# Performance work log

Measured on AMD Instinct MI355X. Metric: run time of the kernel, lower is better.

Reference implementation:

```python
import jax, jax.numpy as jnp
import numpy as np
from jax.scipy.linalg import expm

UNITS = 128  # input last dim = UNITS + 1 (state + time column)


def setup_inputs() -> dict:
    key = jax.random.key(0)
    k1, k2 = jax.random.split(key)
    # [B, units+1]: first `units` cols are the state x, last col is time t
    inputs = jax.random.uniform(k1, (4096, UNITS + 1), dtype=jnp.float32)
    # posterior sample w of size 2*units-1 (diag params + skew params)
    params = jax.random.normal(k2, (2 * UNITS - 1,), dtype=jnp.float32)
    return {"inputs": inputs, "params": params}


def _vec_to_K(params, units):
    # sigma = -softplus(p[:units])**2  -> (negative) diagonal of generator
    sigma = -jax.nn.softplus(params[:units]) ** 2
    # ceta = -p[units:2*units-1]      -> skew super/sub-diagonal
    ceta = -params[units:2 * units - 1]
    # K = diag(sigma) + M - M^T where M = pad(diag(ceta)) is the superdiagonal
    return jnp.diag(sigma) + jnp.diag(ceta, 1) - jnp.diag(ceta, -1)


def reference(inputs, params):
    units = inputs.shape[-1] - 1
    K = _vec_to_K(params, units)                       # [n, n]
    t = inputs[..., -1]                                # [B]
    # kernel_b = expm(t_b * K)  -> batched matrix exponential [B, n, n]
    kernel = jax.vmap(expm)(t[:, None, None] * K)
    # out_b = x_b @ kernel_b
    out = jnp.einsum('bn,bnm->bm', inputs[..., :units], kernel)
    return out
```

## Files before the change

kernel.cpp:

```cpp
#include <hip/hip_runtime.h>
#include <math.h>

#define UNITS 128


__global__ __launch_bounds__(256) void expv_kernel(
    const float* __restrict__ inputs,
    const float* __restrict__ params,
    float* __restrict__ out,
    int B)
{
    const int gid  = blockIdx.x * blockDim.x + threadIdx.x;
    const int wave = gid >> 6;
    const int lane = gid & 63;
    if (wave >= B) return;

    const int i0 = lane * 2;

    const float p0 = params[i0];
    const float p1 = params[i0 + 1];
    const float sp0 = fmaxf(p0, 0.f) + log1pf(expf(-fabsf(p0)));
    const float sp1 = fmaxf(p1, 0.f) + log1pf(expf(-fabsf(p1)));
    const float sig0 = -sp0 * sp0;
    const float sig1 = -sp1 * sp1;
    const float ce0 = -params[UNITS + i0];
    const float ce1 = (lane < 63) ? -params[UNITS + i0 + 1] : 0.f;
    const float ced = (lane > 0)  ? -params[UNITS + i0 - 1] : 0.f;

    const float* row = inputs + (size_t)wave * (UNITS + 1);
    const float x0 = row[i0];
    const float x1 = row[i0 + 1];
    const float t  = row[UNITS];

    const float a0 = t * sig0;
    const float a1 = t * sig1;
    const float c0 = t * ce0;
    const float c1 = t * ce1;
    const float cd = t * ced;

    float r = fmaxf(fabsf(a0) + fabsf(c0) + fabsf(cd),
                    fabsf(a1) + fabsf(c1) + fabsf(c0));
    #pragma unroll
    for (int off = 32; off >= 1; off >>= 1)
        r = fmaxf(r, __shfl_xor(r, off, 64));

    int s = (int)ceilf(r);
    s = (s < 1) ? 1 : ((s > 64) ? 64 : s);
    const float inv_s = 1.0f / (float)s;

    float w0 = x0, w1 = x1;
    for (int step = 0; step < s; ++step) {
        float q0 = w0, q1 = w1;
        float acc0 = w0, acc1 = w1;
        #pragma unroll
        for (int k = 1; k <= 10; ++k) {
            const float qdn = __shfl_up(q1, 1, 64);
            const float qup = __shfl_down(q0, 1, 64);
            const float f = inv_s * (1.0f / (float)k);
            const float n0 = (a0 * q0 - c0 * q1 + cd * qdn) * f;
            const float n1 = (a1 * q1 - c1 * qup + c0 * q0) * f;
            q0 = n0; q1 = n1;
            acc0 += q0; acc1 += q1;
        }
        w0 = acc0; w1 = acc1;
    }

    float2* orow = (float2*)(out + (size_t)wave * UNITS);
    orow[lane] = make_float2(w0, w1);
}

extern "C" void kernel_launch(void* const* d_in, const int* in_sizes, int n_in,
                              void* d_out, int out_size, void* d_ws, size_t ws_size,
                              hipStream_t stream) {
    const float* inputs = (const float*)d_in[0];
    const float* params = (const float*)d_in[1];
    float* out = (float*)d_out;

    const int B = in_sizes[0] / (UNITS + 1);
    const int waves_per_block = 4;
    const int block = 64 * waves_per_block;
    const int grid  = (B + waves_per_block - 1) / waves_per_block;

    expv_kernel<<<grid, block, 0, stream>>>(inputs, params, out, B);
}
```

Measured before the change: 14.05 us.

## Batch two rows per wave and raise Taylor degree to cut scaling steps

Each wave now processes two batch rows, computing the parameter-dependent generator terms and norm reduction once and interleaving two independent Taylor recurrences for more instruction-level parallelism. The Taylor degree rises from 10 to 16 and the step count is chosen from norm/4 instead of norm, which reduces the number of substeps. The per-step scale factor is also folded into the coefficients. The trade-off is more shuffles and FLOPs per step, twice the register use per lane, half as many waves in flight, and a shared step count based on the larger t of the two rows.

```diff
diff --git a/kernel.cpp b/kernel.cpp
--- a/kernel.cpp
+++ b/kernel.cpp
@@ -2,6 +2,8 @@
 #include <math.h>
 
 #define UNITS 128
+#define THETA 4.0f
+#define MDEG  16
 
 
 __global__ __launch_bounds__(256) void expv_kernel(
@@ -13,7 +15,10 @@
     const int gid  = blockIdx.x * blockDim.x + threadIdx.x;
     const int wave = gid >> 6;
     const int lane = gid & 63;
-    if (wave >= B) return;
+    const int eA   = wave * 2;
+    if (eA >= B) return;
+    const int  eB   = eA + 1;
+    const bool hasB = (eB < B);
 
     const int i0 = lane * 2;
 
@@ -27,46 +32,57 @@
     const float ce1 = (lane < 63) ? -params[UNITS + i0 + 1] : 0.f;
     const float ced = (lane > 0)  ? -params[UNITS + i0 - 1] : 0.f;
 
-    const float* row = inputs + (size_t)wave * (UNITS + 1);
-    const float x0 = row[i0];
-    const float x1 = row[i0 + 1];
-    const float t  = row[UNITS];
-
-    const float a0 = t * sig0;
-    const float a1 = t * sig1;
-    const float c0 = t * ce0;
-    const float c1 = t * ce1;
-    const float cd = t * ced;
-
-    float r = fmaxf(fabsf(a0) + fabsf(c0) + fabsf(cd),
-                    fabsf(a1) + fabsf(c1) + fabsf(c0));
+    float rm = fmaxf(fabsf(sig0) + fabsf(ce0) + fabsf(ced),
+                     fabsf(sig1) + fabsf(ce1) + fabsf(ce0));
     #pragma unroll
     for (int off = 32; off >= 1; off >>= 1)
-        r = fmaxf(r, __shfl_xor(r, off, 64));
+        rm = fmaxf(rm, __shfl_xor(rm, off, 64));
 
-    int s = (int)ceilf(r);
+    const float* rowA = inputs + (size_t)eA * (UNITS + 1);
+    const float* rowB = inputs + (size_t)(hasB ? eB : eA) * (UNITS + 1);
+    const float x0A = rowA[i0], x1A = rowA[i0 + 1], tA = rowA[UNITS];
+    const float x0B = rowB[i0], x1B = rowB[i0 + 1], tB = rowB[UNITS];
+
+    const float r = rm * fmaxf(tA, tB);
+    int s = (int)ceilf(r / THETA);
     s = (s < 1) ? 1 : ((s > 64) ? 64 : s);
     const float inv_s = 1.0f / (float)s;
 
-    float w0 = x0, w1 = x1;
+    const float fA = tA * inv_s, fB = tB * inv_s;
+    const float a0A = sig0 * fA, a1A = sig1 * fA;
+    const float c0A = ce0 * fA,  c1A = ce1 * fA,  cdA = ced * fA;
+    const float a0B = sig0 * fB, a1B = sig1 * fB;
+    const float c0B = ce0 * fB,  c1B = ce1 * fB,  cdB = ced * fB;
+
+    float w0A = x0A, w1A = x1A;
+    float w0B = x0B, w1B = x1B;
     for (int step = 0; step < s; ++step) {
-        float q0 = w0, q1 = w1;
-        float acc0 = w0, acc1 = w1;
+        float q0A = w0A, q1A = w1A, acc0A = w0A, acc1A = w1A;
+        float q0B = w0B, q1B = w1B, acc0B = w0B, acc1B = w1B;
         #pragma unroll
-        for (int k = 1; k <= 10; ++k) {
-            const float qdn = __shfl_up(q1, 1, 64);
-            const float qup = __shfl_down(q0, 1, 64);
-            const float f = inv_s * (1.0f / (float)k);
-            const float n0 = (a0 * q0 - c0 * q1 + cd * qdn) * f;
-            const float n1 = (a1 * q1 - c1 * qup + c0 * q0) * f;
-            q0 = n0; q1 = n1;
-            acc0 += q0; acc1 += q1;
+        for (int k = 1; k <= MDEG; ++k) {
+            const float dA = __shfl_up  (q1A, 1, 64);
+            const float uA = __shfl_down(q0A, 1, 64);
+            const float dB = __shfl_up  (q1B, 1, 64);
+            const float uB = __shfl_down(q0B, 1, 64);
+            const float ck = 1.0f / (float)k;
+            const float n0A = (a0A * q0A - c0A * q1A + cdA * dA) * ck;
+            const float n1A = (a1A * q1A - c1A * uA  + c0A * q0A) * ck;
+            const float n0B = (a0B * q0B - c0B * q1B + cdB * dB) * ck;
+            const float n1B = (a1B * q1B - c1B * uB  + c0B * q0B) * ck;
+            q0A = n0A; q1A = n1A; acc0A += q0A; acc1A += q1A;
+            q0B = n0B; q1B = n1B; acc0B += q0B; acc1B += q1B;
         }
-        w0 = acc0; w1 = acc1;
+        w0A = acc0A; w1A = acc1A;
+        w0B = acc0B; w1B = acc1B;
     }
 
-    float2* orow = (float2*)(out + (size_t)wave * UNITS);
-    orow[lane] = make_float2(w0, w1);
+    float2* orA = (float2*)(out + (size_t)eA * UNITS);
+    orA[lane] = make_float2(w0A, w1A);
+    if (hasB) {
+        float2* orB = (float2*)(out + (size_t)eB * UNITS);
+        orB[lane] = make_float2(w0B, w1B);
+    }
 }
 
 extern "C" void kernel_launch(void* const* d_in, const int* in_sizes, int n_in,
@@ -77,9 +93,9 @@
     float* out = (float*)d_out;
 
     const int B = in_sizes[0] / (UNITS + 1);
+    const int n_waves = (B + 1) / 2;
     const int waves_per_block = 4;
-    const int block = 64 * waves_per_block;
-    const int grid  = (B + waves_per_block - 1) / waves_per_block;
+    const int grid = (n_waves + waves_per_block - 1) / waves_per_block;
 
-    expv_kernel<<<grid, block, 0, stream>>>(inputs, params, out, B);
+    expv_kernel<<<grid, 64 * waves_per_block, 0, stream>>>(inputs, params, out, B);
 }
```

Measured after the change: 11.43 us. -18.6%, faster.
